# Performance work log

Measured on AMD Instinct MI355X. Metric: run time of the kernel, lower is better.

## Reference

```python
import jax, jax.numpy as jnp
import numpy as np

K = 4          # Chebyshev order
N = 8192       # nodes
I = 128        # input_size
H = 256        # hidden_size
E = 262144     # nnz in Laplacian


def _uniform(key, shape, bound):
    return jax.random.uniform(key, shape, jnp.float32, -bound, bound)


def setup_inputs() -> dict:
    key = jax.random.key(0)
    ks = jax.random.split(key, 20)
    bound = np.sqrt(1.0 / I)
    inp = {
        "x": jax.random.normal(ks[0], (N, I), jnp.float32),
        "h": jax.random.normal(ks[1], (N, H), jnp.float32),
        "c": jax.random.normal(ks[2], (N, H), jnp.float32),
        "lap_vals": 0.1 * jax.random.normal(ks[3], (E,), jnp.float32),
        "pos": jax.random.randint(ks[4], (E, 2), 0, N, jnp.int64),
        "W_fh": _uniform(ks[5], (K, H, H), bound),
        "W_fx": _uniform(ks[6], (K, H, I), bound),
        "bf": _uniform(ks[7], (N, H), bound),
        "W_ih": _uniform(ks[8], (K, H, H), bound),
        "W_ix": _uniform(ks[9], (K, H, I), bound),
        "bi": _uniform(ks[10], (N, H), bound),
        "W_oh": _uniform(ks[11], (K, H, H), bound),
        "W_ox": _uniform(ks[12], (K, H, I), bound),
        "bo": _uniform(ks[13], (N, H), bound),
        "W_ch": _uniform(ks[14], (K, H, H), bound),
        "W_cx": _uniform(ks[15], (K, H, I), bound),
        "bc": _uniform(ks[16], (N, H), bound),
    }
    return inp


def cheb_features(L, X):
    # T_k(L) @ X via the 3-term recurrence applied to vectors (no N x N powers).
    Ts = [X, L @ X]
    for _ in range(2, K):
        Ts.append(2.0 * (L @ Ts[-1]) - Ts[-2])
    return jnp.stack(Ts[:K])  # [K, N, F]


def graph_conv(TX, W):
    # sum_k T_k(L) X W_k^T ; TX: [K,N,F], W: [K,H,F] -> [N,H]
    return jnp.einsum("knf,khf->nh", TX, W)


def reference(x, h, c, lap_vals, pos, W_fh, W_fx, bf, W_ih, W_ix, bi,
              W_oh, W_ox, bo, W_ch, W_cx, bc):
    L = jnp.zeros((N, N), jnp.float32).at[pos[:, 0], pos[:, 1]].set(lap_vals)
    Th = cheb_features(L, h)  # [K,N,H]
    Tx = cheb_features(L, x)  # [K,N,I]
    f = jax.nn.sigmoid(graph_conv(Th, W_fh) + graph_conv(Tx, W_fx) + bf)
    i = jax.nn.sigmoid(graph_conv(Th, W_ih) + graph_conv(Tx, W_ix) + bi)
    o = jax.nn.sigmoid(graph_conv(Th, W_oh) + graph_conv(Tx, W_ox) + bo)
    c_new = i * jnp.tanh(graph_conv(Th, W_ch) + graph_conv(Tx, W_cx) + bc) + f * c
    h_new = o * jnp.tanh(c_new)
    return (h_new, c_new)
```

## Files before the change

kernel.cpp:

```cpp
#include <hip/hip_runtime.h>
#include <hip/hip_bf16.h>
#include <cstdint>

#define NN 8192
#define HH 256
#define II 128
#define KORD 4
#define EE 262144
#define KW 1536
#define MW 1024
#define RCAP 128

typedef __attribute__((ext_vector_type(8))) short bf16x8;
typedef __attribute__((ext_vector_type(8))) unsigned short u16x8;
typedef __attribute__((ext_vector_type(4))) float f32x4;

__device__ __forceinline__ float bf2f(unsigned short u) {
    union { uint32_t i; float f; } x; x.i = ((uint32_t)u) << 16; return x.f;
}
__device__ __forceinline__ unsigned short f2bf(float f) {
    __hip_bfloat16 b = __float2bfloat16(f);
    return *(unsigned short*)&b;
}

__device__ __forceinline__ void read_pos(const int* __restrict__ pos, int flag,
                                         int e, int& r, int& c) {
    if (flag) { r = pos[4 * e]; c = pos[4 * e + 2]; }
    else      { r = pos[2 * e]; c = pos[2 * e + 1]; }
}

__global__ void init_small(uint32_t* __restrict__ rcnt,
                           const int* __restrict__ pos, int* __restrict__ flag) {
    int i = blockIdx.x * blockDim.x + threadIdx.x;
    if (i < NN) rcnt[i] = 0u;
    if (i == 0) {
        int f = 1;
        for (int k = 0; k < 128; ++k) {
            if (pos[2 * k + 1] != 0) { f = 0; break; }
        }
        *flag = f;
    }
}

__global__ void scatter_fixed(const int* __restrict__ pos, const int* __restrict__ flagp,
                              const float* __restrict__ lap,
                              uint32_t* __restrict__ rcnt, uint2* __restrict__ cpack) {
    int e = blockIdx.x * blockDim.x + threadIdx.x;
    if (e >= EE) return;
    int flag = *flagp;
    int r, c; read_pos(pos, flag, e, r, c);
    uint32_t slot = atomicAdd(&rcnt[r], 1u);
    if (slot < RCAP) {
        uint2 p;
        p.x = ((uint32_t)(e + 1) << 13) | (uint32_t)c;
        p.y = __float_as_uint(lap[e]);
        cpack[(size_t)r * RCAP + slot] = p;
    }
}

__global__ __launch_bounds__(256) void dedup_rows(uint32_t* __restrict__ rcnt,
                                                  uint2* __restrict__ cpack) {
    int r = blockIdx.x * 4 + (threadIdx.x >> 6);
    int lane = threadIdx.x & 63;
    uint32_t lenu = rcnt[r];
    int len = (lenu > RCAP) ? RCAP : (int)lenu;
    uint2* base = &cpack[(size_t)r * RCAP];
    uint32_t m0 = 0u, m1 = 0u;
    if (lane < len) m0 = base[lane].x;
    if (64 + lane < len) m1 = base[64 + lane].x;
    bool lose0 = false, lose1 = false;
    int nchunk = (len + 63) >> 6;
    for (int ch = 0; ch < nchunk; ++ch) {
        int cl = len - ch * 64; if (cl > 64) cl = 64;
        for (int i = 0; i < cl; ++i) {
            uint32_t mi = __shfl(ch == 0 ? m0 : m1, i);
            lose0 |= (((mi ^ m0) & 8191u) == 0u) && (mi > m0);
            lose1 |= (((mi ^ m1) & 8191u) == 0u) && (mi > m1);
        }
    }
    if (lane < len) {
        base[lane].x = m0 & 8191u;
        if (lose0) base[lane].y = 0u;
    }
    if (64 + lane < len) {
        base[64 + lane].x = m1 & 8191u;
        if (lose1) base[64 + lane].y = 0u;
    }
    if (lane == 0 && lenu > RCAP) rcnt[r] = RCAP;
}

template <int F, bool LAST>
__device__ __forceinline__ void spmv_seg(
    const uint32_t* __restrict__ rcnt, const uint2* __restrict__ cp,
    const unsigned short* __restrict__ Xb, const unsigned short* __restrict__ Pb,
    unsigned short* __restrict__ Yb, unsigned short* __restrict__ Am, int colbase,
    float a, float b, int r, int lane) {
    uint32_t len = rcnt[r]; if (len > RCAP) len = RCAP;
    uint32_t s = (uint32_t)r * RCAP, e = s + len;
    int off = lane * 8;
    float acc[8];
#pragma unroll
    for (int j = 0; j < 8; ++j) acc[j] = 0.0f;
    uint32_t i = s;
    for (; i + 4 <= e; i += 4) {
        uint2 p0 = cp[i], p1 = cp[i + 1], p2 = cp[i + 2], p3 = cp[i + 3];
        u16x8 g0 = *(const u16x8*)&Xb[(size_t)p0.x * F + off];
        u16x8 g1 = *(const u16x8*)&Xb[(size_t)p1.x * F + off];
        u16x8 g2 = *(const u16x8*)&Xb[(size_t)p2.x * F + off];
        u16x8 g3 = *(const u16x8*)&Xb[(size_t)p3.x * F + off];
        float v0 = __uint_as_float(p0.y), v1 = __uint_as_float(p1.y);
        float v2 = __uint_as_float(p2.y), v3 = __uint_as_float(p3.y);
#pragma unroll
        for (int j = 0; j < 8; ++j)
            acc[j] += v0 * bf2f(g0[j]) + v1 * bf2f(g1[j]) +
                      v2 * bf2f(g2[j]) + v3 * bf2f(g3[j]);
    }
    for (; i < e; ++i) {
        uint2 p0 = cp[i];
        u16x8 g0 = *(const u16x8*)&Xb[(size_t)p0.x * F + off];
        float v0 = __uint_as_float(p0.y);
#pragma unroll
        for (int j = 0; j < 8; ++j) acc[j] += v0 * bf2f(g0[j]);
    }
    u16x8 ob;
    if (b != 0.0f) {
        u16x8 pv = *(const u16x8*)&Pb[(size_t)r * F + off];
#pragma unroll
        for (int j = 0; j < 8; ++j) ob[j] = f2bf(a * acc[j] + b * bf2f(pv[j]));
    } else {
#pragma unroll
        for (int j = 0; j < 8; ++j) ob[j] = f2bf(a * acc[j]);
    }
    if (!LAST) *(u16x8*)&Yb[(size_t)r * F + off] = ob;
    *(u16x8*)&Am[(size_t)r * KW + colbase + off] = ob;
}

#define NBH (NN / 8)
#define NBX (NN / 16)
template <bool LAST>
__global__ __launch_bounds__(256) void spmv_cheb_dual(
    const uint32_t* __restrict__ rcnt, const uint2* __restrict__ cp,
    const unsigned short* __restrict__ Xh, const unsigned short* __restrict__ Ph,
    unsigned short* __restrict__ Yh, int cbh,
    const unsigned short* __restrict__ Xx, const unsigned short* __restrict__ Px,
    unsigned short* __restrict__ Yx, int cbx,
    unsigned short* __restrict__ Am, float a, float b) {
    int bid = blockIdx.x, t = threadIdx.x;
    if (bid < NBH) {
        int r = bid * 8 + (t >> 5), lane = t & 31;
        spmv_seg<HH, LAST>(rcnt, cp, Xh, Ph, Yh, Am, cbh, a, b, r, lane);
    } else {
        int r = (bid - NBH) * 16 + (t >> 4), lane = t & 15;
        spmv_seg<II, LAST>(rcnt, cp, Xx, Px, Yx, Am, cbx, a, b, r, lane);
    }
}

__global__ void pack_T0(const float* __restrict__ h, const float* __restrict__ x,
                        unsigned short* __restrict__ Hb, unsigned short* __restrict__ Xb,
                        unsigned short* __restrict__ Am) {
    int idx = blockIdx.x * blockDim.x + threadIdx.x;
    if (idx >= NN * 96) return;
    int n, q, col;
    const float* src;
    unsigned short* st;
    if (idx < NN * 64) { n = idx >> 6; q = (idx & 63) * 4; src = &h[(size_t)n * HH + q]; st = &Hb[(size_t)n * HH + q]; col = q; }
    else { int ix = idx - NN * 64; n = ix >> 5; q = (ix & 31) * 4; src = &x[(size_t)n * II + q]; st = &Xb[(size_t)n * II + q]; col = 1024 + q; }
    float4 v = *(const float4*)src;
    ushort4 pk;
    pk.x = f2bf(v.x); pk.y = f2bf(v.y); pk.z = f2bf(v.z); pk.w = f2bf(v.w);
    *(ushort4*)st = pk;
    *(ushort4*)&Am[(size_t)n * KW + col] = pk;
}

__global__ void pack_B(const float* __restrict__ Wfh, const float* __restrict__ Wih,
                       const float* __restrict__ Woh, const float* __restrict__ Wch,
                       const float* __restrict__ Wfx, const float* __restrict__ Wix,
                       const float* __restrict__ Wox, const float* __restrict__ Wcx,
                       __hip_bfloat16* __restrict__ Bm) {
    int idx = blockIdx.x * blockDim.x + threadIdx.x;
    if (idx >= MW * KW) return;
    int m = idx / KW, j = idx - m * KW;
    int g = m >> 8, hh = m & 255;
    const float* Wh = (g == 0) ? Wfh : (g == 1) ? Wih : (g == 2) ? Woh : Wch;
    const float* Wx = (g == 0) ? Wfx : (g == 1) ? Wix : (g == 2) ? Wox : Wcx;
    float v;
    if (j < 1024) { int k = j >> 8, f = j & 255; v = Wh[((size_t)k * HH + hh) * HH + f]; }
    else { int jj = j - 1024; int k = jj >> 7, f = jj & 127; v = Wx[((size_t)k * HH + hh) * II + f]; }
    Bm[idx] = __float2bfloat16(v);
}

__device__ __forceinline__ void gload_lds16(const void* g, void* l) {
    __builtin_amdgcn_global_load_lds(
        (const __attribute__((address_space(1))) void*)g,
        (__attribute__((address_space(3))) void*)l, 16, 0, 0);
}

__global__ __launch_bounds__(256) void gemm_mfma(
    const __hip_bfloat16* __restrict__ A,
    const __hip_bfloat16* __restrict__ B,
    float* __restrict__ C) {
    __shared__ short Alds[128 * 32];
    __shared__ short Blds[128 * 32];
    int bid = blockIdx.x;
    int sw = (bid & 7) * 64 + (bid >> 3);
    int m0 = (sw & 7) * 128;
    int n0 = (sw >> 3) * 128;
    int t = threadIdx.x;
    int w = t >> 6, l = t & 63;
    int wr = w >> 1, wc = w & 1;
    int lrow = l & 15, lk = (l >> 4) * 8;

    f32x4 acc[4][4];
#pragma unroll
    for (int i = 0; i < 4; ++i)
#pragma unroll
        for (int j = 0; j < 4; ++j) acc[i][j] = (f32x4)0.0f;

    for (int k0 = 0; k0 < KW; k0 += 32) {
#pragma unroll
        for (int s = 0; s < 2; ++s) {
            int e = (s * 256 + t) * 8;
            int row = e >> 5, kk = e & 31;
            gload_lds16(&A[(size_t)(n0 + row) * KW + k0 + kk], &Alds[e]);
            gload_lds16(&B[(size_t)(m0 + row) * KW + k0 + kk], &Blds[e]);
        }
        __syncthreads();
        bf16x8 af[4], bfr[4];
#pragma unroll
        for (int i = 0; i < 4; ++i)
            af[i] = *(const bf16x8*)&Alds[(wr * 64 + i * 16 + lrow) * 32 + lk];
#pragma unroll
        for (int j = 0; j < 4; ++j)
            bfr[j] = *(const bf16x8*)&Blds[(wc * 64 + j * 16 + lrow) * 32 + lk];
#pragma unroll
        for (int i = 0; i < 4; ++i)
#pragma unroll
            for (int j = 0; j < 4; ++j)
                acc[i][j] = __builtin_amdgcn_mfma_f32_16x16x32_bf16(af[i], bfr[j], acc[i][j], 0, 0, 0);
        __syncthreads();
    }

    int r4 = (l >> 4) * 4;
#pragma unroll
    for (int i = 0; i < 4; ++i)
#pragma unroll
        for (int j = 0; j < 4; ++j)
#pragma unroll
            for (int r = 0; r < 4; ++r) {
                int row = n0 + wr * 64 + i * 16 + r4 + r;
                int col = m0 + wc * 64 + j * 16 + lrow;
                C[(size_t)row * MW + col] = acc[i][j][r];
            }
}

__device__ __forceinline__ float sigmoidf_(float x) { return 1.0f / (1.0f + expf(-x)); }

__global__ __launch_bounds__(256) void lstm_ew(
    const float* __restrict__ C,
    const float* __restrict__ bf, const float* __restrict__ bi,
    const float* __restrict__ bo, const float* __restrict__ bc,
    const float* __restrict__ cin, float* __restrict__ out) {
    int i = blockIdx.x * blockDim.x + threadIdx.x;
    if (i >= NN * HH / 4) return;
    int n = i >> 6;
    int h4 = (i & 63) * 4;
    size_t cb = (size_t)n * MW;
    size_t hb = (size_t)n * HH + h4;
    float4 pf = *(const float4*)&C[cb + 0 * HH + h4];
    float4 pi = *(const float4*)&C[cb + 1 * HH + h4];
    float4 po = *(const float4*)&C[cb + 2 * HH + h4];
    float4 pc = *(const float4*)&C[cb + 3 * HH + h4];
    float4 vbf = *(const float4*)&bf[hb];
    float4 vbi = *(const float4*)&bi[hb];
    float4 vbo = *(const float4*)&bo[hb];
    float4 vbc = *(const float4*)&bc[hb];
    float4 vc  = *(const float4*)&cin[hb];
    float4 hn, cn;
    {
        float fg = sigmoidf_(pf.x + vbf.x), ig = sigmoidf_(pi.x + vbi.x);
        float og = sigmoidf_(po.x + vbo.x), cg = tanhf(pc.x + vbc.x);
        cn.x = ig * cg + fg * vc.x; hn.x = og * tanhf(cn.x);
    }
    {
        float fg = sigmoidf_(pf.y + vbf.y), ig = sigmoidf_(pi.y + vbi.y);
        float og = sigmoidf_(po.y + vbo.y), cg = tanhf(pc.y + vbc.y);
        cn.y = ig * cg + fg * vc.y; hn.y = og * tanhf(cn.y);
    }
    {
        float fg = sigmoidf_(pf.z + vbf.z), ig = sigmoidf_(pi.z + vbi.z);
        float og = sigmoidf_(po.z + vbo.z), cg = tanhf(pc.z + vbc.z);
        cn.z = ig * cg + fg * vc.z; hn.z = og * tanhf(cn.z);
    }
    {
        float fg = sigmoidf_(pf.w + vbf.w), ig = sigmoidf_(pi.w + vbi.w);
        float og = sigmoidf_(po.w + vbo.w), cg = tanhf(pc.w + vbc.w);
        cn.w = ig * cg + fg * vc.w; hn.w = og * tanhf(cn.w);
    }
    *(float4*)&out[hb] = hn;
    *(float4*)&out[(size_t)NN * HH + hb] = cn;
}

extern "C" void kernel_launch(void* const* d_in, const int* in_sizes, int n_in,
                              void* d_out, int out_size, void* d_ws, size_t ws_size,
                              hipStream_t stream) {
    const float* x   = (const float*)d_in[0];
    const float* h   = (const float*)d_in[1];
    const float* c   = (const float*)d_in[2];
    const float* lap = (const float*)d_in[3];
    const int*   pos = (const int*)d_in[4];
    const float* Wfh = (const float*)d_in[5];
    const float* Wfx = (const float*)d_in[6];
    const float* bf  = (const float*)d_in[7];
    const float* Wih = (const float*)d_in[8];
    const float* Wix = (const float*)d_in[9];
    const float* bi  = (const float*)d_in[10];
    const float* Woh = (const float*)d_in[11];
    const float* Wox = (const float*)d_in[12];
    const float* bo  = (const float*)d_in[13];
    const float* Wch = (const float*)d_in[14];
    const float* Wcx = (const float*)d_in[15];
    const float* bc  = (const float*)d_in[16];
    float* out = (float*)d_out;

    uint8_t* ws = (uint8_t*)d_ws;
    size_t off = 0;
    auto take = [&](size_t bytes) -> void* {
        void* p = ws + off;
        off += (bytes + 255) & ~(size_t)255;
        return p;
    };
    int*      flag = (int*)take(4);
    uint32_t* rcnt = (uint32_t*)take((size_t)NN * 4);
    uint2*    cpack= (uint2*)take((size_t)NN * RCAP * 8);
    unsigned short* Hb = (unsigned short*)take((size_t)3 * NN * HH * 2);
    unsigned short* Xb = (unsigned short*)take((size_t)3 * NN * II * 2);
    unsigned short* Amat = (unsigned short*)take((size_t)NN * KW * 2);
    __hip_bfloat16* Bmat = (__hip_bfloat16*)take((size_t)MW * KW * 2);
    float*    Cpre = (float*)take((size_t)NN * MW * 4);

    init_small<<<NN / 256, 256, 0, stream>>>(rcnt, pos, flag);
    scatter_fixed<<<EE / 256, 256, 0, stream>>>(pos, flag, lap, rcnt, cpack);
    dedup_rows<<<NN / 4, 256, 0, stream>>>(rcnt, cpack);

    pack_T0<<<(NN * 96 + 255) / 256, 256, 0, stream>>>(h, x, Hb, Xb, Amat);
    pack_B<<<(MW * KW + 255) / 256, 256, 0, stream>>>(Wfh, Wih, Woh, Wch,
                                                      Wfx, Wix, Wox, Wcx, Bmat);

    unsigned short* Hb0 = Hb;
    unsigned short* Hb1 = Hb + (size_t)NN * HH;
    unsigned short* Hb2 = Hb1 + (size_t)NN * HH;
    unsigned short* Xb0 = Xb;
    unsigned short* Xb1 = Xb + (size_t)NN * II;
    unsigned short* Xb2 = Xb1 + (size_t)NN * II;

    int sg = NBH + NBX;
    spmv_cheb_dual<false><<<sg, 256, 0, stream>>>(rcnt, cpack,
        Hb0, Hb0, Hb1, 256, Xb0, Xb0, Xb1, 1152, Amat, 1.0f, 0.0f);
    spmv_cheb_dual<false><<<sg, 256, 0, stream>>>(rcnt, cpack,
        Hb1, Hb0, Hb2, 512, Xb1, Xb0, Xb2, 1280, Amat, 2.0f, -1.0f);
    spmv_cheb_dual<true><<<sg, 256, 0, stream>>>(rcnt, cpack,
        Hb2, Hb1, nullptr, 768, Xb2, Xb1, nullptr, 1408, Amat, 2.0f, -1.0f);

    gemm_mfma<<<512, 256, 0, stream>>>((const __hip_bfloat16*)Amat, Bmat, Cpre);

    lstm_ew<<<(NN * HH / 4 + 255) / 256, 256, 0, stream>>>(Cpre, bf, bi, bo, bc, c, out);
}
```

Measured before the change: 171.8 us.

## Split GEMM K dimension in two and XOR-swizzle LDS tiles

The GEMM now launches a second grid dimension that splits the K=1536 reduction into two halves. Each half writes its own fp32 partial buffer, and the LSTM elementwise kernel sums the two partials before applying the gates. The LDS layout for the A and B tiles is also XOR-swizzled by row to reduce bank conflicts on the fragment reads. The split doubles the block count (1024 blocks) to fill more CUs, at the cost of an extra 32 MB of fp32 partial writes and reads.

```diff
diff --git a/kernel.cpp b/kernel.cpp
--- a/kernel.cpp
+++ b/kernel.cpp
@@ -10,6 +10,8 @@
 #define KW 1536
 #define MW 1024
 #define RCAP 128
+#define KSPLIT 2
+#define KHALF (KW / KSPLIT)
 
 typedef __attribute__((ext_vector_type(8))) short bf16x8;
 typedef __attribute__((ext_vector_type(8))) unsigned short u16x8;
@@ -205,10 +207,13 @@
     int sw = (bid & 7) * 64 + (bid >> 3);
     int m0 = (sw & 7) * 128;
     int n0 = (sw >> 3) * 128;
+    int kz = blockIdx.y;
+    int kbeg = kz * KHALF, kend = kbeg + KHALF;
     int t = threadIdx.x;
     int w = t >> 6, l = t & 63;
     int wr = w >> 1, wc = w & 1;
-    int lrow = l & 15, lk = (l >> 4) * 8;
+    int lrow = l & 15;
+    int sl = (((l >> 4) ^ ((lrow >> 1) & 3)) << 3);
 
     f32x4 acc[4][4];
 #pragma unroll
@@ -216,22 +221,24 @@
 #pragma unroll
         for (int j = 0; j < 4; ++j) acc[i][j] = (f32x4)0.0f;
 
-    for (int k0 = 0; k0 < KW; k0 += 32) {
+    for (int k0 = kbeg; k0 < kend; k0 += 32) {
 #pragma unroll
         for (int s = 0; s < 2; ++s) {
             int e = (s * 256 + t) * 8;
-            int row = e >> 5, kk = e & 31;
-            gload_lds16(&A[(size_t)(n0 + row) * KW + k0 + kk], &Alds[e]);
-            gload_lds16(&B[(size_t)(m0 + row) * KW + k0 + kk], &Blds[e]);
+            int row = e >> 5;
+            int slot = (e >> 3) & 3;
+            int kks = ((slot ^ ((row >> 1) & 3)) << 3);
+            gload_lds16(&A[(size_t)(n0 + row) * KW + k0 + kks], &Alds[e]);
+            gload_lds16(&B[(size_t)(m0 + row) * KW + k0 + kks], &Blds[e]);
         }
         __syncthreads();
         bf16x8 af[4], bfr[4];
 #pragma unroll
         for (int i = 0; i < 4; ++i)
-            af[i] = *(const bf16x8*)&Alds[(wr * 64 + i * 16 + lrow) * 32 + lk];
+            af[i] = *(const bf16x8*)&Alds[(wr * 64 + i * 16 + lrow) * 32 + sl];
 #pragma unroll
         for (int j = 0; j < 4; ++j)
-            bfr[j] = *(const bf16x8*)&Blds[(wc * 64 + j * 16 + lrow) * 32 + lk];
+            bfr[j] = *(const bf16x8*)&Blds[(wc * 64 + j * 16 + lrow) * 32 + sl];
 #pragma unroll
         for (int i = 0; i < 4; ++i)
 #pragma unroll
@@ -240,6 +247,7 @@
         __syncthreads();
     }
 
+    float* Cz = C + (size_t)kz * NN * MW;
     int r4 = (l >> 4) * 4;
 #pragma unroll
     for (int i = 0; i < 4; ++i)
@@ -249,7 +257,7 @@
             for (int r = 0; r < 4; ++r) {
                 int row = n0 + wr * 64 + i * 16 + r4 + r;
                 int col = m0 + wc * 64 + j * 16 + lrow;
-                C[(size_t)row * MW + col] = acc[i][j][r];
+                Cz[(size_t)row * MW + col] = acc[i][j][r];
             }
 }
 
@@ -266,10 +274,19 @@
     int h4 = (i & 63) * 4;
     size_t cb = (size_t)n * MW;
     size_t hb = (size_t)n * HH + h4;
+    const float* C1 = C + (size_t)NN * MW;
     float4 pf = *(const float4*)&C[cb + 0 * HH + h4];
     float4 pi = *(const float4*)&C[cb + 1 * HH + h4];
     float4 po = *(const float4*)&C[cb + 2 * HH + h4];
     float4 pc = *(const float4*)&C[cb + 3 * HH + h4];
+    float4 qf = *(const float4*)&C1[cb + 0 * HH + h4];
+    float4 qi = *(const float4*)&C1[cb + 1 * HH + h4];
+    float4 qo = *(const float4*)&C1[cb + 2 * HH + h4];
+    float4 qc = *(const float4*)&C1[cb + 3 * HH + h4];
+    pf.x += qf.x; pf.y += qf.y; pf.z += qf.z; pf.w += qf.w;
+    pi.x += qi.x; pi.y += qi.y; pi.z += qi.z; pi.w += qi.w;
+    po.x += qo.x; po.y += qo.y; po.z += qo.z; po.w += qo.w;
+    pc.x += qc.x; pc.y += qc.y; pc.z += qc.z; pc.w += qc.w;
     float4 vbf = *(const float4*)&bf[hb];
     float4 vbi = *(const float4*)&bi[hb];
     float4 vbo = *(const float4*)&bo[hb];
@@ -336,7 +353,7 @@
     unsigned short* Xb = (unsigned short*)take((size_t)3 * NN * II * 2);
     unsigned short* Amat = (unsigned short*)take((size_t)NN * KW * 2);
     __hip_bfloat16* Bmat = (__hip_bfloat16*)take((size_t)MW * KW * 2);
-    float*    Cpre = (float*)take((size_t)NN * MW * 4);
+    float*    Cpre = (float*)take((size_t)KSPLIT * NN * MW * 4);
 
     init_small<<<NN / 256, 256, 0, stream>>>(rcnt, pos, flag);
     scatter_fixed<<<EE / 256, 256, 0, stream>>>(pos, flag, lap, rcnt, cpack);
@@ -361,7 +378,8 @@
     spmv_cheb_dual<true><<<sg, 256, 0, stream>>>(rcnt, cpack,
         Hb2, Hb1, nullptr, 768, Xb2, Xb1, nullptr, 1408, Amat, 2.0f, -1.0f);
 
-    gemm_mfma<<<512, 256, 0, stream>>>((const __hip_bfloat16*)Amat, Bmat, Cpre);
+    dim3 gg(512, KSPLIT);
+    gemm_mfma<<<gg, 256, 0, stream>>>((const __hip_bfloat16*)Amat, Bmat, Cpre);
 
     lstm_ew<<<(NN * HH / 4 + 255) / 256, 256, 0, stream>>>(Cpre, bf, bi, bo, bc, c, out);
 }
```

Result: slower. 177.5 us (+3.3%).

## Double-buffer LDS tiles in MFMA GEMM and XOR-swizzle LDS layout

Applied to the files above, without the earlier changes.

The bf16 MFMA GEMM now uses two LDS buffers and issues the global-to-LDS loads for the next K-slice before computing on the current one, so load latency can overlap with MFMA work. It also XOR-swizzles the 16-byte K chunks within each row to cut LDS bank conflicts on the fragment reads. This doubles LDS use per block, which may lower occupancy. It also relies on global_load_lds completing before the single barrier at the end of each iteration.

```diff
diff --git a/kernel.cpp b/kernel.cpp
--- a/kernel.cpp
+++ b/kernel.cpp
@@ -199,8 +199,8 @@
     const __hip_bfloat16* __restrict__ A,
     const __hip_bfloat16* __restrict__ B,
     float* __restrict__ C) {
-    __shared__ short Alds[128 * 32];
-    __shared__ short Blds[128 * 32];
+    __shared__ short Alds[2][128 * 32];
+    __shared__ short Blds[2][128 * 32];
     int bid = blockIdx.x;
     int sw = (bid & 7) * 64 + (bid >> 3);
     int m0 = (sw & 7) * 128;
@@ -208,7 +208,14 @@
     int t = threadIdx.x;
     int w = t >> 6, l = t & 63;
     int wr = w >> 1, wc = w & 1;
-    int lrow = l & 15, lk = (l >> 4) * 8;
+    int lrow = l & 15;
+    int sl = (((l >> 4) ^ ((lrow >> 1) & 3)) << 3);
+
+    int e0 = t * 8;
+    int e1 = (256 + t) * 8;
+    int row0 = e0 >> 5, row1 = e1 >> 5;
+    int kks0 = ((((e0 >> 3) & 3) ^ ((row0 >> 1) & 3)) << 3);
+    int kks1 = ((((e1 >> 3) & 3) ^ ((row1 >> 1) & 3)) << 3);
 
     f32x4 acc[4][4];
 #pragma unroll
@@ -216,29 +223,36 @@
 #pragma unroll
         for (int j = 0; j < 4; ++j) acc[i][j] = (f32x4)0.0f;
 
+#define STAGE(bufi, kk)                                                        \
+    do {                                                                       \
+        gload_lds16(&A[(size_t)(n0 + row0) * KW + (kk) + kks0], &Alds[bufi][e0]); \
+        gload_lds16(&B[(size_t)(m0 + row0) * KW + (kk) + kks0], &Blds[bufi][e0]); \
+        gload_lds16(&A[(size_t)(n0 + row1) * KW + (kk) + kks1], &Alds[bufi][e1]); \
+        gload_lds16(&B[(size_t)(m0 + row1) * KW + (kk) + kks1], &Blds[bufi][e1]); \
+    } while (0)
+
+    STAGE(0, 0);
+    __syncthreads();
+
+    int cur = 0;
     for (int k0 = 0; k0 < KW; k0 += 32) {
-#pragma unroll
-        for (int s = 0; s < 2; ++s) {
-            int e = (s * 256 + t) * 8;
-            int row = e >> 5, kk = e & 31;
-            gload_lds16(&A[(size_t)(n0 + row) * KW + k0 + kk], &Alds[e]);
-            gload_lds16(&B[(size_t)(m0 + row) * KW + k0 + kk], &Blds[e]);
-        }
-        __syncthreads();
+        if (k0 + 32 < KW) STAGE(cur ^ 1, k0 + 32);
         bf16x8 af[4], bfr[4];
 #pragma unroll
         for (int i = 0; i < 4; ++i)
-            af[i] = *(const bf16x8*)&Alds[(wr * 64 + i * 16 + lrow) * 32 + lk];
+            af[i] = *(const bf16x8*)&Alds[cur][(wr * 64 + i * 16 + lrow) * 32 + sl];
 #pragma unroll
         for (int j = 0; j < 4; ++j)
-            bfr[j] = *(const bf16x8*)&Blds[(wc * 64 + j * 16 + lrow) * 32 + lk];
+            bfr[j] = *(const bf16x8*)&Blds[cur][(wc * 64 + j * 16 + lrow) * 32 + sl];
 #pragma unroll
         for (int i = 0; i < 4; ++i)
 #pragma unroll
             for (int j = 0; j < 4; ++j)
                 acc[i][j] = __builtin_amdgcn_mfma_f32_16x16x32_bf16(af[i], bfr[j], acc[i][j], 0, 0, 0);
         __syncthreads();
-    }
+        cur ^= 1;
+    }
+#undef STAGE
 
     int r4 = (l >> 4) * 4;
 #pragma unroll
```

New measurement: 170.8 us. Within noise of the previous version (-0.6%).

## Double-buffer GEMM LDS tiles with BK=64 and XOR-swizzled layout

Applied to the files above, without the earlier changes.

The bf16 MFMA GEMM now stages 128x64 A/B tiles into two LDS buffers, prefetching the next K-slice while computing the current one. Only one barrier per iteration remains instead of two. The LDS layout uses an XOR swizzle of the 16-byte chunk index to avoid bank conflicts on fragment reads. This doubles LDS usage to 64KB per block, which may reduce occupancy.

```diff
diff --git a/kernel.cpp b/kernel.cpp
--- a/kernel.cpp
+++ b/kernel.cpp
@@ -10,6 +10,7 @@
 #define KW 1536
 #define MW 1024
 #define RCAP 128
+#define BK 64
 
 typedef __attribute__((ext_vector_type(8))) short bf16x8;
 typedef __attribute__((ext_vector_type(8))) unsigned short u16x8;
@@ -195,12 +196,23 @@
         (__attribute__((address_space(3))) void*)l, 16, 0, 0);
 }
 
+__device__ __forceinline__ void stage_side(const __hip_bfloat16* __restrict__ G,
+                                           int r0, int kk, int t, short* lds) {
+#pragma unroll
+    for (int s = 0; s < 4; ++s) {
+        int e = (s * 256 + t) * 8;
+        int row = e >> 6;
+        int kks = ((((e >> 3) & 7) ^ (row & 7)) << 3);
+        gload_lds16(&G[(size_t)(r0 + row) * KW + kk + kks], &lds[e]);
+    }
+}
+
 __global__ __launch_bounds__(256) void gemm_mfma(
     const __hip_bfloat16* __restrict__ A,
     const __hip_bfloat16* __restrict__ B,
     float* __restrict__ C) {
-    __shared__ short Alds[128 * 32];
-    __shared__ short Blds[128 * 32];
+    __shared__ short Alds[2][128 * BK];
+    __shared__ short Blds[2][128 * BK];
     int bid = blockIdx.x;
     int sw = (bid & 7) * 64 + (bid >> 3);
     int m0 = (sw & 7) * 128;
@@ -208,7 +220,7 @@
     int t = threadIdx.x;
     int w = t >> 6, l = t & 63;
     int wr = w >> 1, wc = w & 1;
-    int lrow = l & 15, lk = (l >> 4) * 8;
+    int lrow = l & 15, q = l >> 4;
 
     f32x4 acc[4][4];
 #pragma unroll
@@ -216,28 +228,34 @@
 #pragma unroll
         for (int j = 0; j < 4; ++j) acc[i][j] = (f32x4)0.0f;
 
-    for (int k0 = 0; k0 < KW; k0 += 32) {
-#pragma unroll
-        for (int s = 0; s < 2; ++s) {
-            int e = (s * 256 + t) * 8;
-            int row = e >> 5, kk = e & 31;
-            gload_lds16(&A[(size_t)(n0 + row) * KW + k0 + kk], &Alds[e]);
-            gload_lds16(&B[(size_t)(m0 + row) * KW + k0 + kk], &Blds[e]);
+    stage_side(A, n0, 0, t, Alds[0]);
+    stage_side(B, m0, 0, t, Blds[0]);
+    __syncthreads();
+
+    int cur = 0;
+    for (int k0 = 0; k0 < KW; k0 += BK) {
+        if (k0 + BK < KW) {
+            stage_side(A, n0, k0 + BK, t, Alds[cur ^ 1]);
+            stage_side(B, m0, k0 + BK, t, Blds[cur ^ 1]);
+        }
+#pragma unroll
+        for (int h = 0; h < 2; ++h) {
+            int sl = (((h << 2) | q) ^ (lrow & 7)) << 3;
+            bf16x8 af[4], bfr[4];
+#pragma unroll
+            for (int i = 0; i < 4; ++i)
+                af[i] = *(const bf16x8*)&Alds[cur][(wr * 64 + i * 16 + lrow) * BK + sl];
+#pragma unroll
+            for (int j = 0; j < 4; ++j)
+                bfr[j] = *(const bf16x8*)&Blds[cur][(wc * 64 + j * 16 + lrow) * BK + sl];
+#pragma unroll
+            for (int i = 0; i < 4; ++i)
+#pragma unroll
+                for (int j = 0; j < 4; ++j)
+                    acc[i][j] = __builtin_amdgcn_mfma_f32_16x16x32_bf16(af[i], bfr[j], acc[i][j], 0, 0, 0);
         }
         __syncthreads();
-        bf16x8 af[4], bfr[4];
-#pragma unroll
-        for (int i = 0; i < 4; ++i)
-            af[i] = *(const bf16x8*)&Alds[(wr * 64 + i * 16 + lrow) * 32 + lk];
-#pragma unroll
-        for (int j = 0; j < 4; ++j)
-            bfr[j] = *(const bf16x8*)&Blds[(wc * 64 + j * 16 + lrow) * 32 + lk];
-#pragma unroll
-        for (int i = 0; i < 4; ++i)
-#pragma unroll
-            for (int j = 0; j < 4; ++j)
-                acc[i][j] = __builtin_amdgcn_mfma_f32_16x16x32_bf16(af[i], bfr[j], acc[i][j], 0, 0, 0);
-        __syncthreads();
+        cur ^= 1;
     }
 
     int r4 = (l >> 4) * 4;
```

Result: faster. 162.8 us (-5.2%).
